# Kernel optimization log

Measured on AMD Instinct MI355X. Metric: run time of the kernel, lower is better.

The kernel has to match this reference:

```python
import jax, jax.numpy as jnp
import numpy as np

B, S, E = 2, 2048, 1024
H, KV = 16, 4
D = E // H            # head_dim = 64
N_REP = H // KV       # 4
WIN = 256             # window_size
KV_DIM = KV * D       # 256


def setup_inputs() -> dict:
    key = jax.random.key(0)
    ks = jax.random.split(key, 10)
    sc_e = 1.0 / np.sqrt(E)
    return {
        "x":  jax.random.normal(ks[0], (B, S, E), jnp.float32),
        # weights stored as [in, out] (transposed torch Linear weight)
        "wq": jax.random.normal(ks[1], (E, E), jnp.float32) * sc_e,
        "bq": jax.random.normal(ks[2], (E,), jnp.float32) * 0.01,
        "wk": jax.random.normal(ks[3], (E, KV_DIM), jnp.float32) * sc_e,
        "bk": jax.random.normal(ks[4], (KV_DIM,), jnp.float32) * 0.01,
        "wv": jax.random.normal(ks[5], (E, KV_DIM), jnp.float32) * sc_e,
        "bv": jax.random.normal(ks[6], (KV_DIM,), jnp.float32) * 0.01,
        "wo": jax.random.normal(ks[7], (E, E), jnp.float32) * sc_e,
        "bo": jax.random.normal(ks[8], (E,), jnp.float32) * 0.01,
    }


def reference(x, wq, bq, wk, bk, wv, bv, wo, bo):
    b, s, _ = x.shape
    q = (x @ wq + bq).reshape(b, s, H, D).transpose(0, 2, 1, 3)    # [B,H,S,D]
    k = (x @ wk + bk).reshape(b, s, KV, D).transpose(0, 2, 1, 3)   # [B,KV,S,D]
    v = (x @ wv + bv).reshape(b, s, KV, D).transpose(0, 2, 1, 3)
    # repeat_kv: each kv head repeated N_REP times consecutively
    k = jnp.repeat(k, N_REP, axis=1)                               # [B,H,S,D]
    v = jnp.repeat(v, N_REP, axis=1)
    scores = jnp.einsum("bhqd,bhkd->bhqk", q, k) * (D ** -0.5)    # [B,H,S,S]
    i = jnp.arange(s)[:, None]
    j = jnp.arange(s)[None, :]
    masked = (j > i) | ((i - j) > WIN)  # True = masked (causal sliding window)
    scores = jnp.where(masked[None, None], -jnp.inf, scores)
    attn = jax.nn.softmax(scores, axis=-1)
    ctx = jnp.einsum("bhqk,bhkd->bhqd", attn, v)                   # [B,H,S,D]
    ctx = ctx.transpose(0, 2, 1, 3).reshape(b, s, E)
    return ctx @ wo + bo
```

## Files before the change

### kernel.cpp

```cpp
#include <hip/hip_runtime.h>
#include <stdint.h>

typedef unsigned short u16;
typedef __attribute__((ext_vector_type(8))) __bf16 bf16x8;
typedef __attribute__((ext_vector_type(4))) __bf16 bf16x4;
typedef __attribute__((ext_vector_type(4))) float f32x4;

#define S_LEN 2048
#define EMB   1024
#define NH    16
#define NKV   4
#define HD    64
#define WIN   256
#define NB    2
#define MROWS (NB * S_LEN)
#define PPAD  72

__device__ __forceinline__ u16 f2bf(float f) {
    uint32_t u = __float_as_uint(f);
    uint32_t r = (u + 0x7FFFu + ((u >> 16) & 1u)) >> 16;
    return (u16)r;
}

__device__ __forceinline__ float fast_exp2(float x) {
#if __has_builtin(__builtin_amdgcn_exp2f)
    return __builtin_amdgcn_exp2f(x);
#else
    float r; asm("v_exp_f32 %0, %1" : "=v"(r) : "v"(x)); return r;
#endif
}

__device__ __forceinline__ void gload16(const void* g, void* l) {
    __builtin_amdgcn_global_load_lds(
        (const __attribute__((address_space(1))) uint32_t*)(uintptr_t)g,
        (__attribute__((address_space(3))) uint32_t*)(uintptr_t)l,
        16, 0, 0);
}

__device__ __forceinline__ void transpose_job(const float* __restrict__ in,
                                              u16* __restrict__ out,
                                              int R, int C, int bx, int by, int tid) {
    __shared__ float t[32][33];
    int c0 = bx * 32, r0 = by * 32;
    int tx = tid & 31, ty = tid >> 5;
#pragma unroll
    for (int j = 0; j < 32; j += 8)
        t[ty + j][tx] = in[(size_t)(r0 + ty + j) * C + (c0 + tx)];
    __syncthreads();
#pragma unroll
    for (int j = 0; j < 32; j += 8)
        out[(size_t)(c0 + ty + j) * R + (r0 + tx)] = f2bf(t[tx][ty + j]);
}

__global__ __launch_bounds__(256) void prep_kernel(
    const float* __restrict__ x,  const float* __restrict__ wq,
    const float* __restrict__ wk, const float* __restrict__ wv,
    const float* __restrict__ wo,
    u16* __restrict__ xb, u16* __restrict__ wqt, u16* __restrict__ wkt,
    u16* __restrict__ wvt, u16* __restrict__ wot) {
    int bid = blockIdx.x, tid = threadIdx.x;
    if (bid < 2048) {
        int i = bid * 256 + tid;
        const float4* p = (const float4*)x + (size_t)i * 2;
        float4 a = p[0], b = p[1];
        uint4 q;
        q.x = f2bf(a.x) | ((uint32_t)f2bf(a.y) << 16);
        q.y = f2bf(a.z) | ((uint32_t)f2bf(a.w) << 16);
        q.z = f2bf(b.x) | ((uint32_t)f2bf(b.y) << 16);
        q.w = f2bf(b.z) | ((uint32_t)f2bf(b.w) << 16);
        ((uint4*)xb)[i] = q;
    } else if (bid < 3072) {
        int lb = bid - 2048;  transpose_job(wq, wqt, EMB, EMB, lb & 31, lb >> 5, tid);
    } else if (bid < 3328) {
        int lb = bid - 3072;  transpose_job(wk, wkt, EMB, 256, lb & 7, lb >> 3, tid);
    } else if (bid < 3584) {
        int lb = bid - 3328;  transpose_job(wv, wvt, EMB, 256, lb & 7, lb >> 3, tid);
    } else {
        int lb = bid - 3584;  transpose_job(wo, wot, EMB, EMB, lb & 31, lb >> 5, tid);
    }
}

__device__ __forceinline__ void gemm_core64(const __bf16* __restrict__ A, const __bf16* __restrict__ Bt,
                                            int K, int m0, int n0r,
                                            __bf16* As, __bf16* Bs, f32x4 (&acc)[2][4], int tid) {
    const int lane = tid & 63, w = tid >> 6;
    const int wr = w >> 1, wc = w & 1;
    const int r = lane & 15, g = lane >> 4;

    for (int k0 = 0; k0 < K; k0 += 64) {
#pragma unroll
        for (int i = 0; i < 2; ++i) {
            int chunk = (w * 2 + i) * 64 + lane;
            int row = chunk >> 3, cc = chunk & 7;
            gload16(A + (size_t)(m0 + row) * K + k0 + cc * 8, As + chunk * 8);
        }
#pragma unroll
        for (int i = 0; i < 4; ++i) {
            int chunk = (w * 4 + i) * 64 + lane;
            int row = chunk >> 3, cc = chunk & 7;
            gload16(Bt + (size_t)(n0r + row) * K + k0 + cc * 8, Bs + chunk * 8);
        }
        __syncthreads();
        bf16x8 af[2][2], bfr[4][2];
#pragma unroll
        for (int mf = 0; mf < 2; ++mf)
#pragma unroll
            for (int kk = 0; kk < 2; ++kk)
                af[mf][kk] = *(const bf16x8*)(As + (wr * 32 + mf * 16 + r) * 64 + kk * 32 + g * 8);
#pragma unroll
        for (int nf = 0; nf < 4; ++nf)
#pragma unroll
            for (int kk = 0; kk < 2; ++kk)
                bfr[nf][kk] = *(const bf16x8*)(Bs + (wc * 64 + nf * 16 + r) * 64 + kk * 32 + g * 8);
#pragma unroll
        for (int mf = 0; mf < 2; ++mf)
#pragma unroll
            for (int nf = 0; nf < 4; ++nf)
#pragma unroll
                for (int kk = 0; kk < 2; ++kk)
                    acc[mf][nf] = __builtin_amdgcn_mfma_f32_16x16x32_bf16(
                        af[mf][kk], bfr[nf][kk], acc[mf][nf], 0, 0, 0);
        __syncthreads();
    }
}

__global__ __launch_bounds__(256, 4) void gemm_qkv_kernel(
    const __bf16* __restrict__ xb, const __bf16* __restrict__ wqt,
    const __bf16* __restrict__ wkt, const __bf16* __restrict__ wvt,
    const float* __restrict__ bq, const float* __restrict__ bk, const float* __restrict__ bv,
    __bf16* __restrict__ Qb, __bf16* __restrict__ Kb, __bf16* __restrict__ Vblk) {
    __shared__ __align__(16) __bf16 As[64 * 64];
    __shared__ __align__(16) __bf16 Bs[128 * 64];
    int tid = threadIdx.x;
    int n0 = blockIdx.x * 128, m0 = blockIdx.y * 64;

    const __bf16* Bt; int n0r; const float* bias; int mode;
    if (n0 < 1024)      { Bt = wqt; n0r = n0;        bias = bq; mode = 0; }
    else if (n0 < 1280) { Bt = wkt; n0r = n0 - 1024; bias = bk; mode = 1; }
    else                { Bt = wvt; n0r = n0 - 1280; bias = bv; mode = 2; }

    f32x4 acc[2][4];
    f32x4 z = {0.f, 0.f, 0.f, 0.f};
#pragma unroll
    for (int i = 0; i < 2; ++i)
#pragma unroll
        for (int j = 0; j < 4; ++j) acc[i][j] = z;

    gemm_core64(xb, Bt, EMB, m0, n0r, As, Bs, acc, tid);

    const int lane = tid & 63, w = tid >> 6;
    const int wr = w >> 1, wc = w & 1, r = lane & 15, g = lane >> 4;
#pragma unroll
    for (int nf = 0; nf < 4; ++nf) {
        int nn = n0r + wc * 64 + nf * 16 + r;
        float bb = bias[nn];
        int hh = nn >> 6, dd = nn & 63;
        if (mode == 2) {
#pragma unroll
            for (int mf = 0; mf < 2; ++mf) {
                int s0 = m0 + wr * 32 + mf * 16 + g * 4;
                int bi = s0 >> 11, s = s0 & 2047;
                bf16x4 pk;
#pragma unroll
                for (int reg = 0; reg < 4; ++reg) pk[reg] = (__bf16)(acc[mf][nf][reg] + bb);
                *reinterpret_cast<bf16x4*>(Vblk + (size_t)(bi * NKV + hh) * (S_LEN * HD)
                                           + (s >> 6) * 4096 + dd * 64 + (s & 63)) = pk;
            }
        } else {
#pragma unroll
            for (int mf = 0; mf < 2; ++mf)
#pragma unroll
                for (int reg = 0; reg < 4; ++reg) {
                    int m = m0 + wr * 32 + mf * 16 + g * 4 + reg;
                    int bi = m >> 11, s = m & 2047;
                    __bf16 o = (__bf16)(acc[mf][nf][reg] + bb);
                    if (mode == 0)
                        Qb[((size_t)(bi * NH + hh) * S_LEN + s) * HD + dd] = o;
                    else
                        Kb[((size_t)(bi * NKV + hh) * S_LEN + s) * HD + dd] = o;
                }
        }
    }
}

__global__ __launch_bounds__(256, 3) void attn_kernel(const __bf16* __restrict__ Qb,
                                                      const __bf16* __restrict__ Kb,
                                                      const __bf16* __restrict__ Vblk,
                                                      __bf16* __restrict__ ctx) {
    __shared__ __align__(16) __bf16 Ks[2][64 * 64];
    __shared__ __align__(16) __bf16 Vs[2][64 * 64];
    __shared__ __align__(16) __bf16 Plds[4][16 * PPAD];
    const int tid = threadIdx.x;
    const int lane = tid & 63, w = tid >> 6;
    const int r = lane & 15, g = lane >> 4;
    const int q0 = blockIdx.x * 64;
    const int h = blockIdx.y, b = blockIdx.z;
    const int kvh = h >> 2;
    const __bf16* Qw = Qb + ((size_t)(b * NH + h) * S_LEN + q0 + w * 16) * HD;
    const __bf16* Kh = Kb + (size_t)(b * NKV + kvh) * S_LEN * HD;
    const __bf16* Vh = Vblk + (size_t)(b * NKV + kvh) * S_LEN * HD;
    __bf16* Pw = &Plds[w][0];

    const int n0s = w * 128 + lane;
    const int n1s = n0s + 64;
    const int srcoff0 = (n0s >> 3) * 64 + (((n0s & 7) ^ ((n0s >> 3) & 7)) * 8);
    const int srcoff1 = (n1s >> 3) * 64 + (((n1s & 7) ^ ((n1s >> 3) & 7)) * 8);
    const int dst0 = (w * 2) * 512;
    const int dst1 = dst0 + 512;

    auto stage = [&](int buf, int kbase) {
        const __bf16* Kt = Kh + (size_t)kbase * 64;
        const __bf16* Vt = Vh + (size_t)kbase * 64;
        gload16(Kt + srcoff0, &Ks[buf][dst0]);
        gload16(Kt + srcoff1, &Ks[buf][dst1]);
        gload16(Vt + srcoff0, &Vs[buf][dst0]);
        gload16(Vt + srcoff1, &Vs[buf][dst1]);
    };

    const int swz0 = ((0 * 4 + g) ^ (r & 7)) * 8;
    const int swz1 = ((1 * 4 + g) ^ (r & 7)) * 8;

    bf16x8 qf[2];
#pragma unroll
    for (int kk = 0; kk < 2; ++kk)
        qf[kk] = *(const bf16x8*)(Qw + r * 64 + kk * 32 + g * 8);

    f32x4 z = {0.f, 0.f, 0.f, 0.f};
    f32x4 o[4];
#pragma unroll
    for (int i = 0; i < 4; ++i) o[i] = z;
    float psum = 0.f;

    const float SC = 0.18033688011112042f;
    const int iq = q0 + w * 16 + r;

    auto tile = [&](int buf, int kbase, bool masked) {
        const __bf16* Kl = &Ks[buf][0];
        const __bf16* Vl = &Vs[buf][0];
        bf16x8 kf[4][2];
#pragma unroll
        for (int nf = 0; nf < 4; ++nf) {
            kf[nf][0] = *(const bf16x8*)(Kl + nf * 1024 + r * 64 + swz0);
            kf[nf][1] = *(const bf16x8*)(Kl + nf * 1024 + r * 64 + swz1);
        }
        f32x4 sa[4];
#pragma unroll
        for (int nf = 0; nf < 4; ++nf) sa[nf] = z;
#pragma unroll
        for (int nf = 0; nf < 4; ++nf)
#pragma unroll
            for (int kk = 0; kk < 2; ++kk)
                sa[nf] = __builtin_amdgcn_mfma_f32_16x16x32_bf16(kf[nf][kk], qf[kk], sa[nf], 0, 0, 0);
#pragma unroll
        for (int nf = 0; nf < 4; ++nf) {
            int jb = kbase + nf * 16 + g * 4;
            bf16x4 pk;
#pragma unroll
            for (int reg = 0; reg < 4; ++reg) {
                float x = sa[nf][reg] * SC;
                if (masked) {
                    uint32_t d = (uint32_t)(iq - (jb + reg));
                    x = (d <= (uint32_t)WIN) ? x : -1e30f;
                }
                float e = fast_exp2(x);
                psum += e;
                pk[reg] = (__bf16)e;
            }
            *reinterpret_cast<bf16x4*>(Pw + r * PPAD + nf * 16 + g * 4) = pk;
        }
        bf16x8 vf[4][2];
#pragma unroll
        for (int nf2 = 0; nf2 < 4; ++nf2) {
            vf[nf2][0] = *(const bf16x8*)(Vl + nf2 * 1024 + r * 64 + swz0);
            vf[nf2][1] = *(const bf16x8*)(Vl + nf2 * 1024 + r * 64 + swz1);
        }
#pragma unroll
        for (int kk2 = 0; kk2 < 2; ++kk2) {
            bf16x8 pa = *(const bf16x8*)(Pw + r * PPAD + kk2 * 32 + g * 8);
#pragma unroll
            for (int nf2 = 0; nf2 < 4; ++nf2)
                o[nf2] = __builtin_amdgcn_mfma_f32_16x16x32_bf16(vf[nf2][kk2], pa, o[nf2], 0, 0, 0);
        }
    };

    const int kb0 = (q0 >= 256) ? (q0 - 256) : 0;
    const int nt = (q0 - kb0) / 64 + 1;
    stage(0, kb0);
    __syncthreads();
    for (int t = 0; t < nt; ++t) {
        int kbase = kb0 + t * 64;
        if (t + 1 < nt) stage((t + 1) & 1, kbase + 64);
        bool masked = (kbase == q0) || (q0 >= 256 && t == 0);
        tile(t & 1, kbase, masked);
        __syncthreads();
    }

    psum += __shfl_xor(psum, 16, 64);
    psum += __shfl_xor(psum, 32, 64);
    float linv = 1.0f / psum;

    int s = q0 + w * 16 + r;
#pragma unroll
    for (int nf2 = 0; nf2 < 4; ++nf2) {
        bf16x4 pk;
#pragma unroll
        for (int reg = 0; reg < 4; ++reg) pk[reg] = (__bf16)(o[nf2][reg] * linv);
        *reinterpret_cast<bf16x4*>(ctx + ((size_t)(b * S_LEN + s)) * EMB + h * 64 + nf2 * 16 + g * 4) = pk;
    }
}

__global__ __launch_bounds__(256, 4) void gemm_out_kernel(const __bf16* __restrict__ ctxb,
                                                          const __bf16* __restrict__ wot,
                                                          const float* __restrict__ bo,
                                                          float* __restrict__ out) {
    __shared__ __align__(16) __bf16 As[64 * 64];
    __shared__ __align__(16) __bf16 Bs[128 * 64];
    int tid = threadIdx.x;
    int n0 = blockIdx.x * 128, m0 = blockIdx.y * 64;

    f32x4 acc[2][4];
    f32x4 z = {0.f, 0.f, 0.f, 0.f};
#pragma unroll
    for (int i = 0; i < 2; ++i)
#pragma unroll
        for (int j = 0; j < 4; ++j) acc[i][j] = z;

    gemm_core64(ctxb, wot, EMB, m0, n0, As, Bs, acc, tid);

    const int lane = tid & 63, w = tid >> 6;
    const int wr = w >> 1, wc = w & 1, r = lane & 15, g = lane >> 4;
#pragma unroll
    for (int nf = 0; nf < 4; ++nf) {
        int n = n0 + wc * 64 + nf * 16 + r;
        float bb = bo[n];
#pragma unroll
        for (int mf = 0; mf < 2; ++mf)
#pragma unroll
            for (int reg = 0; reg < 4; ++reg) {
                int m = m0 + wr * 32 + mf * 16 + g * 4 + reg;
                out[(size_t)m * EMB + n] = acc[mf][nf][reg] + bb;
            }
    }
}

extern "C" void kernel_launch(void* const* d_in, const int* in_sizes, int n_in,
                              void* d_out, int out_size, void* d_ws, size_t ws_size,
                              hipStream_t stream) {
    const float* x  = (const float*)d_in[0];
    const float* wq = (const float*)d_in[1];
    const float* bq = (const float*)d_in[2];
    const float* wk = (const float*)d_in[3];
    const float* bk = (const float*)d_in[4];
    const float* wv = (const float*)d_in[5];
    const float* bv = (const float*)d_in[6];
    const float* wo = (const float*)d_in[7];
    const float* bo = (const float*)d_in[8];
    float* out = (float*)d_out;

    char* ws = (char*)d_ws;
    __bf16* xb   = (__bf16*)ws;          ws += (size_t)MROWS * EMB * 2;
    __bf16* wqt  = (__bf16*)ws;          ws += (size_t)EMB * EMB * 2;
    __bf16* wkt  = (__bf16*)ws;          ws += (size_t)256 * EMB * 2;
    __bf16* wvt  = (__bf16*)ws;          ws += (size_t)256 * EMB * 2;
    __bf16* wot  = (__bf16*)ws;          ws += (size_t)EMB * EMB * 2;
    __bf16* Qb   = (__bf16*)ws;          ws += (size_t)NB * NH * S_LEN * HD * 2;
    __bf16* Kb   = (__bf16*)ws;          ws += (size_t)NB * NKV * S_LEN * HD * 2;
    __bf16* Vblk = (__bf16*)ws;          ws += (size_t)NB * NKV * S_LEN * HD * 2;
    __bf16* ctx  = (__bf16*)ws;          ws += (size_t)MROWS * EMB * 2;

    prep_kernel<<<4608, 256, 0, stream>>>(x, wq, wk, wv, wo,
                                          (u16*)xb, (u16*)wqt, (u16*)wkt, (u16*)wvt, (u16*)wot);
    gemm_qkv_kernel<<<dim3(12, 64), 256, 0, stream>>>(xb, wqt, wkt, wvt, bq, bk, bv, Qb, Kb, Vblk);
    attn_kernel<<<dim3(32, 16, 2), 256, 0, stream>>>(Qb, Kb, Vblk, ctx);
    gemm_out_kernel<<<dim3(8, 64), 256, 0, stream>>>(ctx, wot, bo, out);
}
```

Measured before the change: 74.10 us.

## Double-buffer GEMM LDS tiles, remap workgroups across XCDs, widen weight transpose stores

The GEMM core now double-buffers the A and B LDS tiles, issuing global-to-LDS loads for the next K step before computing the current one, so load latency overlaps with MFMA work. Both GEMM kernels use a 1D grid with a blockIdx remap that groups consecutive tiles per XCD for better L2 locality. The weight transpose now handles 64x32 tiles and writes packed 32-bit bf16 pairs, which halves the number of prep blocks. The extra LDS lowers the occupancy bound from 4 to 3. The loop also keeps a single barrier per iteration, so correctness depends on the gload-to-LDS writes into the other buffer not racing with reads from the previous iteration.

```diff
diff --git a/kernel.cpp b/kernel.cpp
--- a/kernel.cpp
+++ b/kernel.cpp
@@ -37,19 +37,22 @@
         16, 0, 0);
 }
 
-__device__ __forceinline__ void transpose_job(const float* __restrict__ in,
-                                              u16* __restrict__ out,
-                                              int R, int C, int bx, int by, int tid) {
-    __shared__ float t[32][33];
-    int c0 = bx * 32, r0 = by * 32;
+__device__ __forceinline__ void transpose_job64(const float* __restrict__ in,
+                                                u16* __restrict__ out,
+                                                int R, int C, int bx, int by, int tid) {
+    __shared__ float t[64][33];
+    int c0 = bx * 32, r0 = by * 64;
     int tx = tid & 31, ty = tid >> 5;
 #pragma unroll
-    for (int j = 0; j < 32; j += 8)
+    for (int j = 0; j < 64; j += 8)
         t[ty + j][tx] = in[(size_t)(r0 + ty + j) * C + (c0 + tx)];
     __syncthreads();
 #pragma unroll
-    for (int j = 0; j < 32; j += 8)
-        out[(size_t)(c0 + ty + j) * R + (r0 + tx)] = f2bf(t[tx][ty + j]);
+    for (int j = 0; j < 32; j += 8) {
+        int c = j + ty;
+        uint32_t v = f2bf(t[2 * tx][c]) | ((uint32_t)f2bf(t[2 * tx + 1][c]) << 16);
+        *(uint32_t*)(out + (size_t)(c0 + c) * R + r0 + 2 * tx) = v;
+    }
 }
 
 __global__ __launch_bounds__(256) void prep_kernel(
@@ -69,49 +72,56 @@
         q.z = f2bf(b.x) | ((uint32_t)f2bf(b.y) << 16);
         q.w = f2bf(b.z) | ((uint32_t)f2bf(b.w) << 16);
         ((uint4*)xb)[i] = q;
-    } else if (bid < 3072) {
-        int lb = bid - 2048;  transpose_job(wq, wqt, EMB, EMB, lb & 31, lb >> 5, tid);
-    } else if (bid < 3328) {
-        int lb = bid - 3072;  transpose_job(wk, wkt, EMB, 256, lb & 7, lb >> 3, tid);
-    } else if (bid < 3584) {
-        int lb = bid - 3328;  transpose_job(wv, wvt, EMB, 256, lb & 7, lb >> 3, tid);
+    } else if (bid < 2560) {
+        int lb = bid - 2048;  transpose_job64(wq, wqt, EMB, EMB, lb & 31, lb >> 5, tid);
+    } else if (bid < 2688) {
+        int lb = bid - 2560;  transpose_job64(wk, wkt, EMB, 256, lb & 7, lb >> 3, tid);
+    } else if (bid < 2816) {
+        int lb = bid - 2688;  transpose_job64(wv, wvt, EMB, 256, lb & 7, lb >> 3, tid);
     } else {
-        int lb = bid - 3584;  transpose_job(wo, wot, EMB, EMB, lb & 31, lb >> 5, tid);
+        int lb = bid - 2816;  transpose_job64(wo, wot, EMB, EMB, lb & 31, lb >> 5, tid);
     }
 }
 
 __device__ __forceinline__ void gemm_core64(const __bf16* __restrict__ A, const __bf16* __restrict__ Bt,
                                             int K, int m0, int n0r,
-                                            __bf16* As, __bf16* Bs, f32x4 (&acc)[2][4], int tid) {
+                                            __bf16 (*As)[64 * 64], __bf16 (*Bs)[128 * 64],
+                                            f32x4 (&acc)[2][4], int tid) {
     const int lane = tid & 63, w = tid >> 6;
     const int wr = w >> 1, wc = w & 1;
     const int r = lane & 15, g = lane >> 4;
 
-    for (int k0 = 0; k0 < K; k0 += 64) {
+    auto stage = [&](int buf, int k0) {
 #pragma unroll
         for (int i = 0; i < 2; ++i) {
             int chunk = (w * 2 + i) * 64 + lane;
             int row = chunk >> 3, cc = chunk & 7;
-            gload16(A + (size_t)(m0 + row) * K + k0 + cc * 8, As + chunk * 8);
+            gload16(A + (size_t)(m0 + row) * K + k0 + cc * 8, &As[buf][(w * 2 + i) * 512]);
         }
 #pragma unroll
         for (int i = 0; i < 4; ++i) {
             int chunk = (w * 4 + i) * 64 + lane;
             int row = chunk >> 3, cc = chunk & 7;
-            gload16(Bt + (size_t)(n0r + row) * K + k0 + cc * 8, Bs + chunk * 8);
-        }
-        __syncthreads();
+            gload16(Bt + (size_t)(n0r + row) * K + k0 + cc * 8, &Bs[buf][(w * 4 + i) * 512]);
+        }
+    };
+
+    stage(0, 0);
+    __syncthreads();
+    for (int k0 = 0; k0 < K; k0 += 64) {
+        int cur = (k0 >> 6) & 1;
+        if (k0 + 64 < K) stage(cur ^ 1, k0 + 64);
         bf16x8 af[2][2], bfr[4][2];
 #pragma unroll
         for (int mf = 0; mf < 2; ++mf)
 #pragma unroll
             for (int kk = 0; kk < 2; ++kk)
-                af[mf][kk] = *(const bf16x8*)(As + (wr * 32 + mf * 16 + r) * 64 + kk * 32 + g * 8);
+                af[mf][kk] = *(const bf16x8*)(&As[cur][(wr * 32 + mf * 16 + r) * 64 + kk * 32 + g * 8]);
 #pragma unroll
         for (int nf = 0; nf < 4; ++nf)
 #pragma unroll
             for (int kk = 0; kk < 2; ++kk)
-                bfr[nf][kk] = *(const bf16x8*)(Bs + (wc * 64 + nf * 16 + r) * 64 + kk * 32 + g * 8);
+                bfr[nf][kk] = *(const bf16x8*)(&Bs[cur][(wc * 64 + nf * 16 + r) * 64 + kk * 32 + g * 8]);
 #pragma unroll
         for (int mf = 0; mf < 2; ++mf)
 #pragma unroll
@@ -124,15 +134,16 @@
     }
 }
 
-__global__ __launch_bounds__(256, 4) void gemm_qkv_kernel(
+__global__ __launch_bounds__(256, 3) void gemm_qkv_kernel(
     const __bf16* __restrict__ xb, const __bf16* __restrict__ wqt,
     const __bf16* __restrict__ wkt, const __bf16* __restrict__ wvt,
     const float* __restrict__ bq, const float* __restrict__ bk, const float* __restrict__ bv,
     __bf16* __restrict__ Qb, __bf16* __restrict__ Kb, __bf16* __restrict__ Vblk) {
-    __shared__ __align__(16) __bf16 As[64 * 64];
-    __shared__ __align__(16) __bf16 Bs[128 * 64];
+    __shared__ __align__(16) __bf16 As[2][64 * 64];
+    __shared__ __align__(16) __bf16 Bs[2][128 * 64];
     int tid = threadIdx.x;
-    int n0 = blockIdx.x * 128, m0 = blockIdx.y * 64;
+    int wg = (blockIdx.x & 7) * 96 + (blockIdx.x >> 3);
+    int n0 = (wg % 12) * 128, m0 = (wg / 12) * 64;
 
     const __bf16* Bt; int n0r; const float* bias; int mode;
     if (n0 < 1024)      { Bt = wqt; n0r = n0;        bias = bq; mode = 0; }
@@ -309,14 +320,15 @@
     }
 }
 
-__global__ __launch_bounds__(256, 4) void gemm_out_kernel(const __bf16* __restrict__ ctxb,
+__global__ __launch_bounds__(256, 3) void gemm_out_kernel(const __bf16* __restrict__ ctxb,
                                                           const __bf16* __restrict__ wot,
                                                           const float* __restrict__ bo,
                                                           float* __restrict__ out) {
-    __shared__ __align__(16) __bf16 As[64 * 64];
-    __shared__ __align__(16) __bf16 Bs[128 * 64];
+    __shared__ __align__(16) __bf16 As[2][64 * 64];
+    __shared__ __align__(16) __bf16 Bs[2][128 * 64];
     int tid = threadIdx.x;
-    int n0 = blockIdx.x * 128, m0 = blockIdx.y * 64;
+    int wg = (blockIdx.x & 7) * 64 + (blockIdx.x >> 3);
+    int n0 = (wg % 8) * 128, m0 = (wg / 8) * 64;
 
     f32x4 acc[2][4];
     f32x4 z = {0.f, 0.f, 0.f, 0.f};
@@ -368,9 +380,9 @@
     __bf16* Vblk = (__bf16*)ws;          ws += (size_t)NB * NKV * S_LEN * HD * 2;
     __bf16* ctx  = (__bf16*)ws;          ws += (size_t)MROWS * EMB * 2;
 
-    prep_kernel<<<4608, 256, 0, stream>>>(x, wq, wk, wv, wo,
+    prep_kernel<<<3328, 256, 0, stream>>>(x, wq, wk, wv, wo,
                                           (u16*)xb, (u16*)wqt, (u16*)wkt, (u16*)wvt, (u16*)wot);
-    gemm_qkv_kernel<<<dim3(12, 64), 256, 0, stream>>>(xb, wqt, wkt, wvt, bq, bk, bv, Qb, Kb, Vblk);
+    gemm_qkv_kernel<<<768, 256, 0, stream>>>(xb, wqt, wkt, wvt, bq, bk, bv, Qb, Kb, Vblk);
     attn_kernel<<<dim3(32, 16, 2), 256, 0, stream>>>(Qb, Kb, Vblk, ctx);
-    gemm_out_kernel<<<dim3(8, 64), 256, 0, stream>>>(ctx, wot, bo, out);
-}
+    gemm_out_kernel<<<512, 256, 0, stream>>>(ctx, wot, bo, out);
+}
```

New measurement: 66.51 us. -10.2%, faster.
